# Kernel tuning notes

Hardware: AMD Instinct MI355X
Metric: run time of the kernel (lower is better)

Reference implementation:

```python
import jax, jax.numpy as jnp
import numpy as np

B, D_IN, D_H, D_OUT, E = 4096, 1024, 4096, 1024, 8
N_ACTIVE = 5              # max(1, int(8 * 0.625))
TEMP = float(np.e)        # BoltzmannGate default temperature
N_CAMP_A = E // 2


def setup_inputs() -> dict:
    key = jax.random.key(0)
    ks = jax.random.split(key, 6)
    s_in = 1.0 / np.sqrt(D_IN)
    s_h = 1.0 / np.sqrt(D_H)
    return {
        "x": jax.random.normal(ks[0], (B, D_IN), jnp.float32),
        "gate_w": jax.random.normal(ks[1], (D_IN, E), jnp.float32) * s_in,
        "gate_b": jnp.zeros((E,), jnp.float32),
        "w1": jax.random.normal(ks[2], (E, D_IN, D_H), jnp.float32) * s_in,
        "b1": jnp.zeros((E, D_H), jnp.float32),
        "w2": jax.random.normal(ks[3], (E, D_H, D_OUT), jnp.float32) * s_h,
        "b2": jnp.zeros((E, D_OUT), jnp.float32),
        "ph_alpha": jnp.array(1.0, jnp.float32),
        "ph_beta": jnp.array(0.0, jnp.float32),
    }


def _forward(x, gate_w, gate_b, w1, b1, w2, b2, ph_alpha, ph_beta):
    # BoltzmannGate: softmax over temperature-scaled scores, top-k mask, renorm
    scores = (x @ gate_w + gate_b) / TEMP                 # [B, E]
    probs = jax.nn.softmax(scores, axis=-1)
    _, topk_idx = jax.lax.top_k(probs, N_ACTIVE)          # [B, k]
    rows = jnp.arange(x.shape[0])[:, None]
    mask = jnp.zeros_like(probs).at[rows, topk_idx].set(1.0)
    w = probs * mask
    weights = w / (w.sum(axis=-1, keepdims=True) + 1e-8)  # [B, E]

    # Dense evaluation of all experts (dropout is inference-mode identity)
    h = jax.nn.relu(jnp.einsum("bi,eih->beh", x, w1) + b1)     # [B, E, H]
    e_out = jnp.einsum("beh,eho->beo", h, w2) + b2             # [B, E, O]

    # Camp A = experts [0, E//2), Camp G = experts [E//2, E)
    out_a = jnp.einsum("be,beo->bo", weights[:, :N_CAMP_A], e_out[:, :N_CAMP_A])
    out_g = jnp.einsum("be,beo->bo", weights[:, N_CAMP_A:], e_out[:, N_CAMP_A:])

    repulsion = out_a - out_g
    # PH distance proxy computed on detached tensors in torch -> stop_gradient
    diff = jax.lax.stop_gradient(repulsion)
    l2 = jnp.linalg.norm(diff, axis=-1)                   # [B]
    var = jnp.var(diff, axis=-1)                          # population var, ddof=0
    ph_dist = l2 * (1.0 + var)
    ph_corr = jax.nn.sigmoid(ph_alpha * ph_dist + ph_beta) * 2.0  # in (0, 2)
    output = repulsion * ph_corr[:, None]
    return output, out_a, out_g


def reference(x, gate_w, gate_b, w1, b1, w2, b2, ph_alpha, ph_beta):
    return _forward(x, gate_w, gate_b, w1, b1, w2, b2, ph_alpha, ph_beta)
```

## Files before the change

kernel.cpp:

```cpp
#include <hip/hip_runtime.h>
#include <hip/hip_bf16.h>
#include <stdint.h>

typedef unsigned short u16;
typedef unsigned int u32;
typedef __attribute__((ext_vector_type(4))) float f32x4;
typedef __attribute__((ext_vector_type(4))) int i32x4;
typedef __attribute__((ext_vector_type(8))) u16 u16x8;
typedef __attribute__((ext_vector_type(8))) __bf16 bf16x8;

constexpr int BATCH = 4096, DIN = 1024, DH = 4096, DOUT = 1024, NEXP = 8;
constexpr int HS_CAP = 2816;

struct Ptr4 { float* p[4]; };

__device__ __forceinline__ u16 f2bf(float f) {
  u32 u = __float_as_uint(f);
  u += 0x7fffu + ((u >> 16) & 1u);
  return (u16)(u >> 16);
}

#define GLOAD_LDS16(gp, lp)                                                    \
  __builtin_amdgcn_global_load_lds(                                           \
      (__attribute__((address_space(1))) void*)(gp),                          \
      (__attribute__((address_space(3))) void*)(lp), 16, 0, 0)

#define BAR()                                                                  \
  { asm volatile("" ::: "memory"); __builtin_amdgcn_s_barrier();               \
    asm volatile("" ::: "memory"); }
#define VM4() asm volatile("s_waitcnt vmcnt(4)" ::: "memory")
#define VM0() asm volatile("s_waitcnt vmcnt(0)" ::: "memory")

#define STG4(q0, q1, kofs, dst)                                                \
  { GLOAD_LDS16((q0) + (kofs), (dst));                                         \
    GLOAD_LDS16((q1) + (kofs), (dst) + 4096); }

__global__ void gate_kernel(const float* __restrict__ x,
                            const float* __restrict__ gw,
                            const float* __restrict__ gb,
                            float* __restrict__ wgt) {
  const int wave = threadIdx.x >> 6, lane = threadIdx.x & 63;
  const int b = blockIdx.x * 4 + wave;
  const float* xr = x + (size_t)b * DIN;
  float acc[NEXP];
#pragma unroll
  for (int e = 0; e < NEXP; ++e) acc[e] = 0.f;
  for (int k = lane; k < DIN; k += 64) {
    const float xv = xr[k];
    const f32x4 g0 = *(const f32x4*)(gw + (size_t)k * NEXP);
    const f32x4 g1 = *(const f32x4*)(gw + (size_t)k * NEXP + 4);
    acc[0] += xv * g0[0]; acc[1] += xv * g0[1];
    acc[2] += xv * g0[2]; acc[3] += xv * g0[3];
    acc[4] += xv * g1[0]; acc[5] += xv * g1[1];
    acc[6] += xv * g1[2]; acc[7] += xv * g1[3];
  }
#pragma unroll
  for (int off = 32; off; off >>= 1)
#pragma unroll
    for (int e = 0; e < NEXP; ++e) acc[e] += __shfl_xor(acc[e], off);
  if (lane == 0) {
    const float invT = 0.36787944117144233f;
    float s[NEXP], mx = -1e30f;
    for (int e = 0; e < NEXP; ++e) { s[e] = (acc[e] + gb[e]) * invT; mx = fmaxf(mx, s[e]); }
    float p[NEXP], sum = 0.f;
    for (int e = 0; e < NEXP; ++e) { p[e] = expf(s[e] - mx); sum += p[e]; }
    const float inv = 1.f / sum;
    for (int e = 0; e < NEXP; ++e) p[e] *= inv;
    float w[NEXP], wsum = 0.f;
    for (int e = 0; e < NEXP; ++e) {
      int cnt = 0;
      for (int j = 0; j < NEXP; ++j) cnt += (p[j] > p[e]) || (p[j] == p[e] && j < e);
      w[e] = (cnt < 5) ? p[e] : 0.f;
      wsum += w[e];
    }
    const float inv2 = 1.f / (wsum + 1e-8f);
    for (int e = 0; e < NEXP; ++e) wgt[(size_t)b * NEXP + e] = w[e] * inv2;
  }
}

__global__ void assign_kernel(const float* __restrict__ wgt,
                              int* __restrict__ cnt, u16* __restrict__ ridx) {
  const int b = blockIdx.x * 256 + threadIdx.x;
#pragma unroll
  for (int e = 0; e < NEXP; ++e) {
    if (wgt[(size_t)b * NEXP + e] != 0.f) {
      const int pos = atomicAdd(&cnt[e], 1);
      if (pos < BATCH) ridx[e * BATCH + pos] = (u16)b;
    }
  }
}

__global__ void gather_cvt(const float* __restrict__ x,
                           const int* __restrict__ cnt,
                           const u16* __restrict__ ridx,
                           u16* __restrict__ Xe) {
  const int e = blockIdx.y, p = blockIdx.x;
  int c = cnt[e]; c = c < HS_CAP ? c : HS_CAP;
  if (p >= c) return;
  const int row = ridx[e * BATCH + p];
  const float* s = x + (size_t)row * DIN;
  u16* d = Xe + ((size_t)e * HS_CAP + p) * DIN;
  const int t = threadIdx.x;
  const f32x4 a = *(const f32x4*)(s + t * 8);
  const f32x4 b = *(const f32x4*)(s + t * 8 + 4);
  u16x8 o;
  o[0] = f2bf(a[0]); o[1] = f2bf(a[1]); o[2] = f2bf(a[2]); o[3] = f2bf(a[3]);
  o[4] = f2bf(b[0]); o[5] = f2bf(b[1]); o[6] = f2bf(b[2]); o[7] = f2bf(b[3]);
  *(u16x8*)(d + t * 8) = o;
}

__global__ void transpose_cvt(const float* __restrict__ src, u16* __restrict__ dst,
                              int C, int ldd, size_t src_slice,
                              size_t dst_hi, size_t dst_lo) {
  __shared__ float ts[64][65];
  const int z = blockIdx.z;
  const float* s = src + (size_t)z * src_slice;
  u16* d = dst + (size_t)(z >> 2) * dst_hi + (size_t)(z & 3) * dst_lo;
  const int c0 = blockIdx.x * 64, r0 = blockIdx.y * 64;
  const int t = threadIdx.x;
  const int lr = t >> 4, lc = (t & 15) * 4;
#pragma unroll
  for (int i = 0; i < 4; ++i) {
    const f32x4 v = *(const f32x4*)(s + (size_t)(r0 + i * 16 + lr) * C + c0 + lc);
    ts[i * 16 + lr][lc] = v[0];
    ts[i * 16 + lr][lc + 1] = v[1];
    ts[i * 16 + lr][lc + 2] = v[2];
    ts[i * 16 + lr][lc + 3] = v[3];
  }
  __syncthreads();
  const int cc = t >> 3, r8 = (t & 7) * 8;
#pragma unroll
  for (int pass = 0; pass < 2; ++pass) {
    const int c = cc + pass * 32;
    u16x8 o;
#pragma unroll
    for (int j = 0; j < 8; ++j) o[j] = f2bf(ts[r8 + j][c]);
    *(u16x8*)(d + (size_t)(c0 + c) * ldd + r0 + r8) = o;
  }
}

__device__ __forceinline__ void rdB4(i32x4 rB[2][2], const char* base, int wc,
                                     int roff, int NH) {
#pragma unroll
  for (int n = 0; n < 2; ++n)
#pragma unroll
    for (int kk = 0; kk < 2; ++kk)
      rB[n][kk] = *(const i32x4*)(base + (((wc * 4 + NH * 2 + n) * 2 + kk) << 10) + roff);
}
template <int MH>
__device__ __forceinline__ void rdA8(i32x4 rA[4][2], const char* base, int wr, int roff) {
#pragma unroll
  for (int m = 0; m < 4; ++m)
#pragma unroll
    for (int kk = 0; kk < 2; ++kk)
      rA[m][kk] = *(const i32x4*)(base + (((wr * 8 + MH * 4 + m) * 2 + kk) << 10) + roff);
}
template <int MH, int NH>
__device__ __forceinline__ void mm16(f32x4 acc[8][4], const i32x4 rA[4][2],
                                     const i32x4 rB[2][2]) {
  __builtin_amdgcn_s_setprio(1);
#pragma unroll
  for (int m = 0; m < 4; ++m)
#pragma unroll
    for (int n = 0; n < 2; ++n)
#pragma unroll
      for (int kk = 0; kk < 2; ++kk)
        acc[MH * 4 + m][NH * 2 + n] = __builtin_amdgcn_mfma_f32_16x16x32_bf16(
            __builtin_bit_cast(bf16x8, rA[m][kk]),
            __builtin_bit_cast(bf16x8, rB[n][kk]),
            acc[MH * 4 + m][NH * 2 + n], 0, 0, 0);
  __builtin_amdgcn_s_setprio(0);
}

#define TILE_BODY(T, CA, CB_, DA_OT, DB_CB)                                    \
  {                                                                            \
    const int t_ = (T);                                                        \
    const bool g1 = (t_ + 1) < NT, g2 = (t_ + 2) < NT;                         \
    const int kA = (t_ + 1) * 64, kB = (t_ + 2) * 64;                          \
    rdA8<0>(rA, CA, wr, roff);                                                 \
    rdB4(rB0, CB_, wc, roff, 0);                                               \
    if (g1) STG4(qA0, qA1, kA, DA_OT);                                         \
    BAR();                                                                     \
    mm16<0, 0>(acc, rA, rB0);                                                  \
    BAR();                                                                     \
    rdB4(rB1, CB_, wc, roff, 1);                                               \
    if (g1) STG4(qA2, qA3, kA, DA_OT + 8192);                                  \
    BAR();                                                                     \
    mm16<0, 1>(acc, rA, rB1);                                                  \
    BAR();                                                                     \
    rdA8<1>(rA, CA, wr, roff);                                                 \
    if (g2) STG4(qB0, qB1, kB, DB_CB);                                         \
    BAR();                                                                     \
    mm16<1, 1>(acc, rA, rB1);                                                  \
    BAR();                                                                     \
    if (g2) {                                                                  \
      STG4(qB2, qB3, kB, DB_CB + 8192);                                        \
      BAR();                                                                   \
      mm16<1, 0>(acc, rA, rB0);                                                \
      VM4();                                                                   \
    } else {                                                                   \
      BAR();                                                                   \
      mm16<1, 0>(acc, rA, rB0);                                                \
      VM0();                                                                   \
    }                                                                          \
    BAR();                                                                     \
  }

template <int EPI>
__global__ __launch_bounds__(512, 2) void gemm256(
    const u16* __restrict__ A0, int lda,
    const u16* __restrict__ Bt0, int ldb, int K,
    u16* __restrict__ dstH0, Ptr4 parts,
    const float* __restrict__ wgt, const float* __restrict__ bias0,
    const int* __restrict__ cnt, const u16* __restrict__ ridx, int camp,
    int NM, int NN) {
  __shared__ __align__(16) u16 sA[2][16384];
  __shared__ __align__(16) u16 sB[2][16384];

  const int tid = threadIdx.x;
  const int w = tid >> 6, lane = tid & 63;
  const int l15 = lane & 15, lh = lane >> 4;
  const int wr = w >> 2, wc = w & 3;

  const int cpx = (int)gridDim.x >> 3;
  const int id = blockIdx.x;
  const int wk = (id & 7) * cpx + (id >> 3);
  const int m = wk % NM;
  const int n = (wk / NM) % NN;
  const int z = wk / (NM * NN);
  const int bM = m * 256, bN = n * 256;

  const int expert = camp * 4 + z;
  int count = cnt[expert];
  count = count < HS_CAP ? count : HS_CAP;
  if (bM >= count) return;
  const int eoff = expert * BATCH;

  const u16* A;
  const u16* Bt;
  const float* bias = bias0;
  u16* dstH = dstH0;
  if (EPI == 0) {
    A = A0 + (size_t)expert * HS_CAP * lda;
    Bt = Bt0 + (size_t)expert * DH * DIN;
    bias = bias0 + (size_t)expert * DH;
    dstH = dstH0 + (size_t)z * HS_CAP * DH;
  } else {
    A = A0 + (size_t)z * HS_CAP * lda;
    Bt = Bt0 + (size_t)z * DH;
  }

  const int lp = lane ^ ((lane & 32) >> 4);
  const int grow = (w >> 1) * 16 + (lp >> 2);
  const int gcol = (w & 1) * 32 + (lp & 3) * 8;

  const u16* qA0 = A + (size_t)(bM + grow) * lda + gcol;
  const u16* qA1 = qA0 + (size_t)64 * lda;
  const u16* qA2 = qA0 + (size_t)128 * lda;
  const u16* qA3 = qA0 + (size_t)192 * lda;
  const u16* qB0 = Bt + (size_t)(bN + grow) * ldb + gcol;
  const u16* qB1 = qB0 + (size_t)64 * ldb;
  const u16* qB2 = qB0 + (size_t)128 * ldb;
  const u16* qB3 = qB0 + (size_t)192 * ldb;

  u16* dA0 = &sA[0][w * 512];
  u16* dA1 = &sA[1][w * 512];
  u16* dB0 = &sB[0][w * 512];
  u16* dB1 = &sB[1][w * 512];

  const int roff = l15 * 64 + ((lh * 16) ^ ((l15 & 8) << 2));
  const char* cA0 = (const char*)&sA[0][0];
  const char* cA1 = (const char*)&sA[1][0];
  const char* cB0 = (const char*)&sB[0][0];
  const char* cB1 = (const char*)&sB[1][0];

  const int NT = K >> 6;
  f32x4 acc[8][4] = {};
  i32x4 rA[4][2], rB0[2][2], rB1[2][2];

  STG4(qB0, qB1, 0, dB0);
  STG4(qB2, qB3, 0, dB0 + 8192);
  STG4(qA0, qA1, 0, dA0);
  STG4(qA2, qA3, 0, dA0 + 8192);
  STG4(qB0, qB1, 64, dB1);
  STG4(qB2, qB3, 64, dB1 + 8192);
  VM4();
  BAR();

  for (int t = 0; t < NT; t += 2) {
    TILE_BODY(t, cA0, cB0, dA1, dB0);
    TILE_BODY(t + 1, cA1, cB1, dA0, dB1);
  }

  if (EPI == 0) {
#pragma unroll
    for (int m2 = 0; m2 < 8; ++m2)
#pragma unroll
      for (int r = 0; r < 4; ++r) {
        const int pos = bM + wr * 128 + m2 * 16 + lh * 4 + r;
        if (pos >= count) continue;
        const int orow = ridx[eoff + pos];
        const float wsc = wgt[(size_t)orow * NEXP + expert];
#pragma unroll
        for (int nn = 0; nn < 4; ++nn) {
          const int col = bN + wc * 64 + nn * 16 + l15;
          float v = acc[m2][nn][r] + bias[col];
          v = fmaxf(v, 0.0f) * wsc;
          dstH[(size_t)pos * DH + col] = f2bf(v);
        }
      }
  } else {
    float* __restrict__ P = parts.p[z];
#pragma unroll
    for (int m2 = 0; m2 < 8; ++m2)
#pragma unroll
      for (int r = 0; r < 4; ++r) {
        const int pos = bM + wr * 128 + m2 * 16 + lh * 4 + r;
        if (pos >= count) continue;
        const int orow = ridx[eoff + pos];
#pragma unroll
        for (int nn = 0; nn < 4; ++nn) {
          const int col = bN + wc * 64 + nn * 16 + l15;
          P[(size_t)orow * DOUT + col] = acc[m2][nn][r];
        }
      }
  }
}

__global__ __launch_bounds__(512, 2) void gemm_combo(
    const u16* __restrict__ Hs0, const u16* __restrict__ w2t0, Ptr4 pc0,
    const u16* __restrict__ Xe, const u16* __restrict__ w1t,
    u16* __restrict__ HsW, const float* __restrict__ b1,
    const float* __restrict__ wgt,
    const int* __restrict__ cnt, const u16* __restrict__ ridx, int l2n) {
  __shared__ __align__(16) u16 sA[2][16384];
  __shared__ __align__(16) u16 sB[2][16384];

  const int tid = threadIdx.x;
  const int w = tid >> 6, lane = tid & 63;
  const int l15 = lane & 15, lh = lane >> 4;
  const int wr = w >> 2, wc = w & 3;

  const bool isL2 = (int)blockIdx.x < l2n;
  const int id = isL2 ? (int)blockIdx.x : (int)blockIdx.x - l2n;
  const int tot = isL2 ? l2n : ((int)gridDim.x - l2n);
  const int cpx = tot >> 3;
  const int wk = (id & 7) * cpx + (id >> 3);
  const int NM = HS_CAP / 256;
  const int NN = isL2 ? (DOUT / 256) : (DH / 256);
  const int m = wk % NM;
  const int n = (wk / NM) % NN;
  const int z = wk / (NM * NN);
  const int bM = m * 256, bN = n * 256;

  const int expert = isL2 ? z : 4 + z;
  int count = cnt[expert];
  count = count < HS_CAP ? count : HS_CAP;
  if (bM >= count) return;
  const int eoff = expert * BATCH;

  const u16* A; const u16* Bt;
  int lda, ldb, K;
  const float* bias = nullptr;
  u16* dstH = nullptr;
  if (isL2) {
    A = Hs0 + (size_t)z * HS_CAP * DH;  lda = DH;
    Bt = w2t0 + (size_t)z * DH;         ldb = 4 * DH;
    K = DH;
  } else {
    A = Xe + (size_t)expert * HS_CAP * DIN;  lda = DIN;
    Bt = w1t + (size_t)expert * DH * DIN;    ldb = DIN;
    K = DIN;
    bias = b1 + (size_t)expert * DH;
    dstH = HsW + (size_t)expert * HS_CAP * DH;
  }

  const int lp = lane ^ ((lane & 32) >> 4);
  const int grow = (w >> 1) * 16 + (lp >> 2);
  const int gcol = (w & 1) * 32 + (lp & 3) * 8;

  const u16* qA0 = A + (size_t)(bM + grow) * lda + gcol;
  const u16* qA1 = qA0 + (size_t)64 * lda;
  const u16* qA2 = qA0 + (size_t)128 * lda;
  const u16* qA3 = qA0 + (size_t)192 * lda;
  const u16* qB0 = Bt + (size_t)(bN + grow) * ldb + gcol;
  const u16* qB1 = qB0 + (size_t)64 * ldb;
  const u16* qB2 = qB0 + (size_t)128 * ldb;
  const u16* qB3 = qB0 + (size_t)192 * ldb;

  u16* dA0 = &sA[0][w * 512];
  u16* dA1 = &sA[1][w * 512];
  u16* dB0 = &sB[0][w * 512];
  u16* dB1 = &sB[1][w * 512];

  const int roff = l15 * 64 + ((lh * 16) ^ ((l15 & 8) << 2));
  const char* cA0 = (const char*)&sA[0][0];
  const char* cA1 = (const char*)&sA[1][0];
  const char* cB0 = (const char*)&sB[0][0];
  const char* cB1 = (const char*)&sB[1][0];

  const int NT = K >> 6;
  f32x4 acc[8][4] = {};
  i32x4 rA[4][2], rB0[2][2], rB1[2][2];

  STG4(qB0, qB1, 0, dB0);
  STG4(qB2, qB3, 0, dB0 + 8192);
  STG4(qA0, qA1, 0, dA0);
  STG4(qA2, qA3, 0, dA0 + 8192);
  STG4(qB0, qB1, 64, dB1);
  STG4(qB2, qB3, 64, dB1 + 8192);
  VM4();
  BAR();

  for (int t = 0; t < NT; t += 2) {
    TILE_BODY(t, cA0, cB0, dA1, dB0);
    TILE_BODY(t + 1, cA1, cB1, dA0, dB1);
  }

  if (isL2) {
    float* __restrict__ P = pc0.p[z];
#pragma unroll
    for (int m2 = 0; m2 < 8; ++m2)
#pragma unroll
      for (int r = 0; r < 4; ++r) {
        const int pos = bM + wr * 128 + m2 * 16 + lh * 4 + r;
        if (pos >= count) continue;
        const int orow = ridx[eoff + pos];
#pragma unroll
        for (int nn = 0; nn < 4; ++nn) {
          const int col = bN + wc * 64 + nn * 16 + l15;
          P[(size_t)orow * DOUT + col] = acc[m2][nn][r];
        }
      }
  } else {
#pragma unroll
    for (int m2 = 0; m2 < 8; ++m2)
#pragma unroll
      for (int r = 0; r < 4; ++r) {
        const int pos = bM + wr * 128 + m2 * 16 + lh * 4 + r;
        if (pos >= count) continue;
        const int orow = ridx[eoff + pos];
        const float wsc = wgt[(size_t)orow * NEXP + expert];
#pragma unroll
        for (int nn = 0; nn < 4; ++nn) {
          const int col = bN + wc * 64 + nn * 16 + l15;
          float v = acc[m2][nn][r] + bias[col];
          v = fmaxf(v, 0.0f) * wsc;
          dstH[(size_t)pos * DH + col] = f2bf(v);
        }
      }
  }
}

__global__ void reduce_kernel(float* __restrict__ dst,
                              const float* __restrict__ p0, const float* __restrict__ p1,
                              const float* __restrict__ p2, const float* __restrict__ p3,
                              const float* __restrict__ wgt,
                              const float* __restrict__ b2c, int camp) {
  const int b = blockIdx.x, t = threadIdx.x;
  const f32x4 wv = *(const f32x4*)(wgt + (size_t)b * NEXP + camp * 4);
  const size_t ro = (size_t)b * DOUT;
#pragma unroll
  for (int j = 0; j < 4; ++j) {
    const int i = j * 256 + t;
    float acc = wv[0] * b2c[i] + wv[1] * b2c[DOUT + i] +
                wv[2] * b2c[2 * DOUT + i] + wv[3] * b2c[3 * DOUT + i];
    acc += (wv[0] != 0.f) ? p0[ro + i] : 0.f;
    acc += (wv[1] != 0.f) ? p1[ro + i] : 0.f;
    acc += (wv[2] != 0.f) ? p2[ro + i] : 0.f;
    acc += (wv[3] != 0.f) ? p3[ro + i] : 0.f;
    dst[ro + i] = acc;
  }
}

__global__ void reduce_final_kernel(float* __restrict__ out,
                                    const float* __restrict__ p0,
                                    const float* __restrict__ p1,
                                    const float* __restrict__ p2,
                                    const float* __restrict__ p3,
                                    const float* __restrict__ wgt,
                                    const float* __restrict__ b2c,
                                    const float* __restrict__ alpha,
                                    const float* __restrict__ beta) {
  const int b = blockIdx.x, t = threadIdx.x;
  const f32x4 wv = *(const f32x4*)(wgt + (size_t)b * NEXP + 4);
  const size_t ro = (size_t)b * DOUT;
  const float* pa = out + (size_t)BATCH * DOUT + ro;
  float* pg = out + (size_t)2 * BATCH * DOUT + ro;
  float* po = out + ro;
  float g[4], d[4], s1 = 0.f, s2 = 0.f;
#pragma unroll
  for (int j = 0; j < 4; ++j) {
    const int i = j * 256 + t;
    float acc = wv[0] * b2c[i] + wv[1] * b2c[DOUT + i] +
                wv[2] * b2c[2 * DOUT + i] + wv[3] * b2c[3 * DOUT + i];
    acc += (wv[0] != 0.f) ? p0[ro + i] : 0.f;
    acc += (wv[1] != 0.f) ? p1[ro + i] : 0.f;
    acc += (wv[2] != 0.f) ? p2[ro + i] : 0.f;
    acc += (wv[3] != 0.f) ? p3[ro + i] : 0.f;
    g[j] = acc;
    d[j] = pa[i] - acc;
    s1 += d[j];
    s2 += d[j] * d[j];
  }
#pragma unroll
  for (int off = 32; off; off >>= 1) {
    s1 += __shfl_xor(s1, off);
    s2 += __shfl_xor(s2, off);
  }
  __shared__ float r1[4], r2[4];
  if ((t & 63) == 0) { r1[t >> 6] = s1; r2[t >> 6] = s2; }
  __syncthreads();
  s1 = r1[0] + r1[1] + r1[2] + r1[3];
  s2 = r2[0] + r2[1] + r2[2] + r2[3];
  const float mean = s1 * (1.f / DOUT);
  const float var = s2 * (1.f / DOUT) - mean * mean;
  const float dist = sqrtf(s2) * (1.f + var);
  const float zz = alpha[0] * dist + beta[0];
  const float corr = 2.f / (1.f + expf(-zz));
#pragma unroll
  for (int j = 0; j < 4; ++j) {
    const int i = j * 256 + t;
    pg[i] = g[j];
    po[i] = d[j] * corr;
  }
}

extern "C" void kernel_launch(void* const* d_in, const int* in_sizes, int n_in,
                              void* d_out, int out_size, void* d_ws, size_t ws_size,
                              hipStream_t stream) {
  const float* x   = (const float*)d_in[0];
  const float* gw  = (const float*)d_in[1];
  const float* gb  = (const float*)d_in[2];
  const float* w1  = (const float*)d_in[3];
  const float* b1  = (const float*)d_in[4];
  const float* w2  = (const float*)d_in[5];
  const float* b2  = (const float*)d_in[6];
  const float* pha = (const float*)d_in[7];
  const float* phb = (const float*)d_in[8];
  float* out = (float*)d_out;
  float* out_a = out + (size_t)BATCH * DOUT;
  float* out_g = out + (size_t)2 * BATCH * DOUT;

  char* ws = (char*)d_ws;
  float* wgt  = (float*)ws;
  int* cnt    = (int*)(ws + 131072);
  u16* ridx   = (u16*)(ws + 135168);
  u16* Xe     = (u16*)(ws + 262144);
  constexpr size_t XE_BYTES  = (size_t)NEXP * HS_CAP * DIN * 2;
  constexpr size_t W1T_BYTES = (size_t)NEXP * DH * DIN * 2;
  constexpr size_t W2T_BYTES = (size_t)DOUT * 4 * DH * 2;
  constexpr size_t P_BYTES   = (size_t)BATCH * DOUT * 4;
  constexpr size_t HS_E      = (size_t)HS_CAP * DH * 2;
  const size_t w1t_off = 262144 + XE_BYTES;
  u16* w1t = (u16*)(ws + w1t_off);

  const size_t pipe_need = w1t_off + W1T_BYTES + 2 * W2T_BYTES + 2 * P_BYTES + 8 * HS_E;
  const size_t merged_need = w1t_off + W1T_BYTES + 2 * P_BYTES + 8 * HS_E;

  constexpr int NM = HS_CAP / 256;
  constexpr int NN1 = DH / 256, NN2 = DOUT / 256;

  gate_kernel<<<BATCH / 4, 256, 0, stream>>>(x, gw, gb, wgt);
  hipMemsetAsync(cnt, 0, NEXP * sizeof(int), stream);
  assign_kernel<<<BATCH / 256, 256, 0, stream>>>(wgt, cnt, ridx);
  gather_cvt<<<dim3(HS_CAP, NEXP), 128, 0, stream>>>(x, cnt, ridx, Xe);
  transpose_cvt<<<dim3(DH / 64, DIN / 64, NEXP), 256, 0, stream>>>(
      w1, w1t, DH, DIN, (size_t)DIN * DH, (size_t)4 * DH * DIN, (size_t)DH * DIN);

  if (ws_size >= pipe_need) {
    u16* w2t0 = (u16*)(ws + w1t_off + W1T_BYTES);
    u16* w2t1 = (u16*)(ws + w1t_off + W1T_BYTES + W2T_BYTES);
    float* P0 = (float*)(ws + w1t_off + W1T_BYTES + 2 * W2T_BYTES);
    float* P1 = (float*)(ws + w1t_off + W1T_BYTES + 2 * W2T_BYTES + P_BYTES);
    u16* Hs   = (u16*)(ws + w1t_off + W1T_BYTES + 2 * W2T_BYTES + 2 * P_BYTES);
    Ptr4 pc0 = {{out_a, out, out_g, P0}};
    Ptr4 pc1 = {{out_g, out, P0, P1}};

    transpose_cvt<<<dim3(DOUT / 64, DH / 64, 4), 256, 0, stream>>>(
        w2, w2t0, DOUT, 4 * DH, (size_t)DH * DOUT, 0, (size_t)DH);
    transpose_cvt<<<dim3(DOUT / 64, DH / 64, 4), 256, 0, stream>>>(
        w2 + (size_t)4 * DH * DOUT, w2t1, DOUT, 4 * DH, (size_t)DH * DOUT, 0, (size_t)DH);

    gemm256<0><<<NM * NN1 * 4, 512, 0, stream>>>(
        Xe, DIN, w1t, DIN, DIN, Hs, pc0, wgt, b1, cnt, ridx, 0, NM, NN1);
    gemm_combo<<<NM * NN2 * 4 + NM * NN1 * 4, 512, 0, stream>>>(
        Hs, w2t0, pc0, Xe, w1t, Hs, b1, wgt, cnt, ridx, NM * NN2 * 4);
    reduce_kernel<<<BATCH, 256, 0, stream>>>(out_a, out_a, out, out_g, P0, wgt, b2, 0);
    gemm256<2><<<NM * NN2 * 4, 512, 0, stream>>>(
        Hs + (size_t)4 * HS_CAP * DH, DH, w2t1, 4 * DH, DH, nullptr, pc1,
        nullptr, nullptr, cnt, ridx, 1, NM, NN2);
    reduce_final_kernel<<<BATCH, 256, 0, stream>>>(out, out_g, out, P0, P1,
                                                   wgt, b2 + (size_t)4 * DOUT,
                                                   pha, phb);
  } else if (ws_size >= merged_need) {
    float* P0 = (float*)(ws + w1t_off + W1T_BYTES);
    float* P1 = (float*)(ws + w1t_off + W1T_BYTES + P_BYTES);
    u16* Hs   = (u16*)(ws + w1t_off + W1T_BYTES + 2 * P_BYTES);
    u16* w2t0 = w1t;
    u16* w2t1 = (u16*)((char*)w1t + W2T_BYTES);
    Ptr4 pc0 = {{out_a, out, out_g, P0}};
    Ptr4 pc1 = {{out_g, out, P0, P1}};

    gemm256<0><<<NM * NN1 * 8, 512, 0, stream>>>(
        Xe, DIN, w1t, DIN, DIN, Hs, pc0, wgt, b1, cnt, ridx, 0, NM, NN1);
    transpose_cvt<<<dim3(DOUT / 64, DH / 64, 4), 256, 0, stream>>>(
        w2, w2t0, DOUT, 4 * DH, (size_t)DH * DOUT, 0, (size_t)DH);
    transpose_cvt<<<dim3(DOUT / 64, DH / 64, 4), 256, 0, stream>>>(
        w2 + (size_t)4 * DH * DOUT, w2t1, DOUT, 4 * DH, (size_t)DH * DOUT, 0, (size_t)DH);
    gemm256<2><<<NM * NN2 * 4, 512, 0, stream>>>(
        Hs, DH, w2t0, 4 * DH, DH, nullptr, pc0, nullptr, nullptr, cnt, ridx, 0, NM, NN2);
    reduce_kernel<<<BATCH, 256, 0, stream>>>(out_a, out_a, out, out_g, P0, wgt, b2, 0);
    gemm256<2><<<NM * NN2 * 4, 512, 0, stream>>>(
        Hs + (size_t)4 * HS_CAP * DH, DH, w2t1, 4 * DH, DH, nullptr, pc1,
        nullptr, nullptr, cnt, ridx, 1, NM, NN2);
    reduce_final_kernel<<<BATCH, 256, 0, stream>>>(out, out_g, out, P0, P1,
                                                   wgt, b2 + (size_t)4 * DOUT,
                                                   pha, phb);
  } else {
    u16* w2t1 = w1t;
    u16* w2t0 = (u16*)(ws + w1t_off + W1T_BYTES);
    float* P0 = (float*)(ws + w1t_off + W1T_BYTES + W2T_BYTES);
    float* P1 = (float*)(ws + w1t_off + W1T_BYTES + W2T_BYTES + P_BYTES);
    u16* Hs   = (u16*)(ws + w1t_off + W1T_BYTES + W2T_BYTES + 2 * P_BYTES);
    Ptr4 pc0 = {{out_a, out, out_g, P0}};
    Ptr4 pc1 = {{out_g, out, P0, P1}};

    transpose_cvt<<<dim3(DOUT / 64, DH / 64, 4), 256, 0, stream>>>(
        w2, w2t0, DOUT, 4 * DH, (size_t)DH * DOUT, 0, (size_t)DH);
    gemm256<0><<<NM * NN1 * 4, 512, 0, stream>>>(
        Xe, DIN, w1t, DIN, DIN, Hs, pc0, wgt, b1, cnt, ridx, 0, NM, NN1);
    transpose_cvt<<<dim3(DOUT / 64, DH / 64, 4), 256, 0, stream>>>(
        w2 + (size_t)4 * DH * DOUT, w2t1, DOUT, 4 * DH, (size_t)DH * DOUT, 0, (size_t)DH);
    gemm256<2><<<NM * NN2 * 4, 512, 0, stream>>>(
        Hs, DH, w2t0, 4 * DH, DH, nullptr, pc0, nullptr, nullptr, cnt, ridx, 0, NM, NN2);
    reduce_kernel<<<BATCH, 256, 0, stream>>>(out_a, out_a, out, out_g, P0, wgt, b2, 0);
    gemm256<0><<<NM * NN1 * 4, 512, 0, stream>>>(
        Xe, DIN, w1t, DIN, DIN, Hs, pc1, wgt, b1, cnt, ridx, 1, NM, NN1);
    gemm256<2><<<NM * NN2 * 4, 512, 0, stream>>>(
        Hs, DH, w2t1, 4 * DH, DH, nullptr, pc1, nullptr, nullptr, cnt, ridx, 1, NM, NN2);
    reduce_final_kernel<<<BATCH, 256, 0, stream>>>(out, out_g, out, P0, P1,
                                                   wgt, b2 + (size_t)4 * DOUT,
                                                   pha, phb);
  }
}
```

Before: 650.8 us.

## Fuse prep stages and overlap weight transposes with GEMMs in heterogeneous launches

Folds expert assignment into the gate kernel and merges the gather/convert with the w1 transpose into one heterogeneous launch. The w2 transpose now runs in the same launch as the layer-1 GEMM, and the camp-A reduce runs alongside the camp-G layer-2 GEMM. The w2 transpose also moves to 512-thread blocks that each handle two tiles, and scratch buffers are remapped onto dead workspace. The goal is fewer launches and filling idle CUs during the GEMM tails, at the cost of more complex block dispatch and heavier LDS use in the transpose blocks.

```diff
diff --git a/kernel.cpp b/kernel.cpp
--- a/kernel.cpp
+++ b/kernel.cpp
@@ -38,7 +38,8 @@
 __global__ void gate_kernel(const float* __restrict__ x,
                             const float* __restrict__ gw,
                             const float* __restrict__ gb,
-                            float* __restrict__ wgt) {
+                            float* __restrict__ wgt,
+                            int* __restrict__ cnt, u16* __restrict__ ridx) {
   const int wave = threadIdx.x >> 6, lane = threadIdx.x & 63;
   const int b = blockIdx.x * 4 + wave;
   const float* xr = x + (size_t)b * DIN;
@@ -68,75 +69,91 @@
     for (int e = 0; e < NEXP; ++e) p[e] *= inv;
     float w[NEXP], wsum = 0.f;
     for (int e = 0; e < NEXP; ++e) {
-      int cnt = 0;
-      for (int j = 0; j < NEXP; ++j) cnt += (p[j] > p[e]) || (p[j] == p[e] && j < e);
-      w[e] = (cnt < 5) ? p[e] : 0.f;
+      int c = 0;
+      for (int j = 0; j < NEXP; ++j) c += (p[j] > p[e]) || (p[j] == p[e] && j < e);
+      w[e] = (c < 5) ? p[e] : 0.f;
       wsum += w[e];
     }
     const float inv2 = 1.f / (wsum + 1e-8f);
-    for (int e = 0; e < NEXP; ++e) wgt[(size_t)b * NEXP + e] = w[e] * inv2;
-  }
-}
-
-__global__ void assign_kernel(const float* __restrict__ wgt,
-                              int* __restrict__ cnt, u16* __restrict__ ridx) {
-  const int b = blockIdx.x * 256 + threadIdx.x;
-#pragma unroll
-  for (int e = 0; e < NEXP; ++e) {
-    if (wgt[(size_t)b * NEXP + e] != 0.f) {
-      const int pos = atomicAdd(&cnt[e], 1);
-      if (pos < BATCH) ridx[e * BATCH + pos] = (u16)b;
+    for (int e = 0; e < NEXP; ++e) {
+      const float wv = w[e] * inv2;
+      wgt[(size_t)b * NEXP + e] = wv;
+      if (wv != 0.f) {
+        const int pos = atomicAdd(&cnt[e], 1);
+        if (pos < BATCH) ridx[e * BATCH + pos] = (u16)b;
+      }
     }
   }
 }
 
-__global__ void gather_cvt(const float* __restrict__ x,
-                           const int* __restrict__ cnt,
-                           const u16* __restrict__ ridx,
-                           u16* __restrict__ Xe) {
-  const int e = blockIdx.y, p = blockIdx.x;
+__device__ __forceinline__ void transpose_pair(
+    const float* __restrict__ src, u16* __restrict__ dst, int C, int ldd,
+    size_t src_slice, size_t dst_hi, size_t dst_lo, int id, int nc2, int nr,
+    float* ts ) {
+  const int tid = threadIdx.x;
+  const int half = tid >> 8, t = tid & 255;
+  const int cp = id % nc2;
+  const int rt = (id / nc2) % nr;
+  const int z = id / (nc2 * nr);
+  const float* s = src + (size_t)z * src_slice;
+  u16* d = dst + (size_t)(z >> 2) * dst_hi + (size_t)(z & 3) * dst_lo;
+  const int c0 = cp * 128 + half * 64, r0 = rt * 64;
+  float* th = ts + half * (64 * 65);
+  const int lr = t >> 4, lc = (t & 15) * 4;
+#pragma unroll
+  for (int i = 0; i < 4; ++i) {
+    const f32x4 v = *(const f32x4*)(s + (size_t)(r0 + i * 16 + lr) * C + c0 + lc);
+    th[(i * 16 + lr) * 65 + lc] = v[0];
+    th[(i * 16 + lr) * 65 + lc + 1] = v[1];
+    th[(i * 16 + lr) * 65 + lc + 2] = v[2];
+    th[(i * 16 + lr) * 65 + lc + 3] = v[3];
+  }
+  __syncthreads();
+  const int cc = t >> 3, r8 = (t & 7) * 8;
+#pragma unroll
+  for (int pass = 0; pass < 2; ++pass) {
+    const int c = cc + pass * 32;
+    u16x8 o;
+#pragma unroll
+    for (int j = 0; j < 8; ++j) o[j] = f2bf(th[(r8 + j) * 65 + c]);
+    *(u16x8*)(d + (size_t)(c0 + c) * ldd + r0 + r8) = o;
+  }
+}
+
+__global__ __launch_bounds__(512) void transpose_pair_kernel(
+    const float* __restrict__ src, u16* __restrict__ dst, int C, int ldd,
+    size_t src_slice, size_t dst_hi, size_t dst_lo, int nc2, int nr) {
+  __shared__ float ts[2][64][65];
+  transpose_pair(src, dst, C, ldd, src_slice, dst_hi, dst_lo, blockIdx.x, nc2,
+                 nr, &ts[0][0][0]);
+}
+
+__global__ __launch_bounds__(512) void prep_hetero(
+    const float* __restrict__ x, const int* __restrict__ cnt,
+    const u16* __restrict__ ridx, u16* __restrict__ Xe,
+    const float* __restrict__ w1, u16* __restrict__ w1t, int gn) {
+  __shared__ float ts[2][64][65];
+  const int id = blockIdx.x;
+  if (id >= gn) {
+    transpose_pair(w1, w1t, DH, DIN, (size_t)DIN * DH, (size_t)4 * DH * DIN,
+                   (size_t)DH * DIN, id - gn, DH / 128, DIN / 64, &ts[0][0][0]);
+    return;
+  }
+  const int tid = threadIdx.x;
+  const int e = id / (HS_CAP / 4);
+  const int p = (id % (HS_CAP / 4)) * 4 + (tid >> 7);
   int c = cnt[e]; c = c < HS_CAP ? c : HS_CAP;
   if (p >= c) return;
   const int row = ridx[e * BATCH + p];
   const float* s = x + (size_t)row * DIN;
   u16* d = Xe + ((size_t)e * HS_CAP + p) * DIN;
-  const int t = threadIdx.x;
+  const int t = tid & 127;
   const f32x4 a = *(const f32x4*)(s + t * 8);
   const f32x4 b = *(const f32x4*)(s + t * 8 + 4);
   u16x8 o;
   o[0] = f2bf(a[0]); o[1] = f2bf(a[1]); o[2] = f2bf(a[2]); o[3] = f2bf(a[3]);
   o[4] = f2bf(b[0]); o[5] = f2bf(b[1]); o[6] = f2bf(b[2]); o[7] = f2bf(b[3]);
   *(u16x8*)(d + t * 8) = o;
-}
-
-__global__ void transpose_cvt(const float* __restrict__ src, u16* __restrict__ dst,
-                              int C, int ldd, size_t src_slice,
-                              size_t dst_hi, size_t dst_lo) {
-  __shared__ float ts[64][65];
-  const int z = blockIdx.z;
-  const float* s = src + (size_t)z * src_slice;
-  u16* d = dst + (size_t)(z >> 2) * dst_hi + (size_t)(z & 3) * dst_lo;
-  const int c0 = blockIdx.x * 64, r0 = blockIdx.y * 64;
-  const int t = threadIdx.x;
-  const int lr = t >> 4, lc = (t & 15) * 4;
-#pragma unroll
-  for (int i = 0; i < 4; ++i) {
-    const f32x4 v = *(const f32x4*)(s + (size_t)(r0 + i * 16 + lr) * C + c0 + lc);
-    ts[i * 16 + lr][lc] = v[0];
-    ts[i * 16 + lr][lc + 1] = v[1];
-    ts[i * 16 + lr][lc + 2] = v[2];
-    ts[i * 16 + lr][lc + 3] = v[3];
-  }
-  __syncthreads();
-  const int cc = t >> 3, r8 = (t & 7) * 8;
-#pragma unroll
-  for (int pass = 0; pass < 2; ++pass) {
-    const int c = cc + pass * 32;
-    u16x8 o;
-#pragma unroll
-    for (int j = 0; j < 8; ++j) o[j] = f2bf(ts[r8 + j][c]);
-    *(u16x8*)(d + (size_t)(c0 + c) * ldd + r0 + r8) = o;
-  }
 }
 
 __device__ __forceinline__ void rdB4(i32x4 rB[2][2], const char* base, int wc,
@@ -206,6 +223,50 @@
     BAR();                                                                     \
   }
 
+#define GEMM_COORDS()                                                          \
+  const int tid = threadIdx.x;                                                 \
+  const int w = tid >> 6, lane = tid & 63;                                     \
+  const int l15 = lane & 15, lh = lane >> 4;                                   \
+  const int wr = w >> 2, wc = w & 3;                                           \
+  const int lp = lane ^ ((lane & 32) >> 4);                                    \
+  const int grow = (w >> 1) * 16 + (lp >> 2);                                  \
+  const int gcol = (w & 1) * 32 + (lp & 3) * 8;                                \
+  const int roff = l15 * 64 + ((lh * 16) ^ ((l15 & 8) << 2));                  \
+  const char* cA0 = (const char*)&sA[0][0];                                    \
+  const char* cA1 = (const char*)&sA[1][0];                                    \
+  const char* cB0 = (const char*)&sB[0][0];                                    \
+  const char* cB1 = (const char*)&sB[1][0];                                    \
+  u16* dA0 = &sA[0][w * 512];                                                  \
+  u16* dA1 = &sA[1][w * 512];                                                  \
+  u16* dB0 = &sB[0][w * 512];                                                  \
+  u16* dB1 = &sB[1][w * 512];
+
+#define GEMM_POINTERS(A, lda, Bt, ldb)                                         \
+  const u16* qA0 = (A) + (size_t)(bM + grow) * (lda) + gcol;                   \
+  const u16* qA1 = qA0 + (size_t)64 * (lda);                                   \
+  const u16* qA2 = qA0 + (size_t)128 * (lda);                                  \
+  const u16* qA3 = qA0 + (size_t)192 * (lda);                                  \
+  const u16* qB0 = (Bt) + (size_t)(bN + grow) * (ldb) + gcol;                  \
+  const u16* qB1 = qB0 + (size_t)64 * (ldb);                                   \
+  const u16* qB2 = qB0 + (size_t)128 * (ldb);                                  \
+  const u16* qB3 = qB0 + (size_t)192 * (ldb);
+
+#define GEMM_RUN()                                                             \
+  f32x4 acc[8][4] = {};                                                        \
+  i32x4 rA[4][2], rB0[2][2], rB1[2][2];                                        \
+  STG4(qB0, qB1, 0, dB0);                                                      \
+  STG4(qB2, qB3, 0, dB0 + 8192);                                               \
+  STG4(qA0, qA1, 0, dA0);                                                      \
+  STG4(qA2, qA3, 0, dA0 + 8192);                                               \
+  STG4(qB0, qB1, 64, dB1);                                                     \
+  STG4(qB2, qB3, 64, dB1 + 8192);                                              \
+  VM4();                                                                       \
+  BAR();                                                                       \
+  for (int t = 0; t < NT; t += 2) {                                            \
+    TILE_BODY(t, cA0, cB0, dA1, dB0);                                          \
+    TILE_BODY(t + 1, cA1, cB1, dA0, dB1);                                      \
+  }
+
 template <int EPI>
 __global__ __launch_bounds__(512, 2) void gemm256(
     const u16* __restrict__ A0, int lda,
@@ -216,11 +277,7 @@
     int NM, int NN) {
   __shared__ __align__(16) u16 sA[2][16384];
   __shared__ __align__(16) u16 sB[2][16384];
-
-  const int tid = threadIdx.x;
-  const int w = tid >> 6, lane = tid & 63;
-  const int l15 = lane & 15, lh = lane >> 4;
-  const int wr = w >> 2, wc = w & 3;
+  GEMM_COORDS();
 
   const int cpx = (int)gridDim.x >> 3;
   const int id = blockIdx.x;
@@ -249,48 +306,9 @@
     A = A0 + (size_t)z * HS_CAP * lda;
     Bt = Bt0 + (size_t)z * DH;
   }
-
-  const int lp = lane ^ ((lane & 32) >> 4);
-  const int grow = (w >> 1) * 16 + (lp >> 2);
-  const int gcol = (w & 1) * 32 + (lp & 3) * 8;
-
-  const u16* qA0 = A + (size_t)(bM + grow) * lda + gcol;
-  const u16* qA1 = qA0 + (size_t)64 * lda;
-  const u16* qA2 = qA0 + (size_t)128 * lda;
-  const u16* qA3 = qA0 + (size_t)192 * lda;
-  const u16* qB0 = Bt + (size_t)(bN + grow) * ldb + gcol;
-  const u16* qB1 = qB0 + (size_t)64 * ldb;
-  const u16* qB2 = qB0 + (size_t)128 * ldb;
-  const u16* qB3 = qB0 + (size_t)192 * ldb;
-
-  u16* dA0 = &sA[0][w * 512];
-  u16* dA1 = &sA[1][w * 512];
-  u16* dB0 = &sB[0][w * 512];
-  u16* dB1 = &sB[1][w * 512];
-
-  const int roff = l15 * 64 + ((lh * 16) ^ ((l15 & 8) << 2));
-  const char* cA0 = (const char*)&sA[0][0];
-  const char* cA1 = (const char*)&sA[1][0];
-  const char* cB0 = (const char*)&sB[0][0];
-  const char* cB1 = (const char*)&sB[1][0];
-
+  GEMM_POINTERS(A, lda, Bt, ldb);
   const int NT = K >> 6;
-  f32x4 acc[8][4] = {};
-  i32x4 rA[4][2], rB0[2][2], rB1[2][2];
-
-  STG4(qB0, qB1, 0, dB0);
-  STG4(qB2, qB3, 0, dB0 + 8192);
-  STG4(qA0, qA1, 0, dA0);
-  STG4(qA2, qA3, 0, dA0 + 8192);
-  STG4(qB0, qB1, 64, dB1);
-  STG4(qB2, qB3, 64, dB1 + 8192);
-  VM4();
-  BAR();
-
-  for (int t = 0; t < NT; t += 2) {
-    TILE_BODY(t, cA0, cB0, dA1, dB0);
-    TILE_BODY(t + 1, cA1, cB1, dA0, dB1);
-  }
+  GEMM_RUN();
 
   if (EPI == 0) {
 #pragma unroll
@@ -327,6 +345,63 @@
   }
 }
 
+__global__ __launch_bounds__(512, 2) void l1_w2t_hetero(
+    const u16* __restrict__ Xe, const u16* __restrict__ w1t,
+    u16* __restrict__ Hs, const float* __restrict__ wgt,
+    const float* __restrict__ b1,
+    const int* __restrict__ cnt, const u16* __restrict__ ridx,
+    const float* __restrict__ w2, u16* __restrict__ w2t0, int l1n) {
+  __shared__ __align__(16) u16 sA[2][16384];
+  __shared__ __align__(16) u16 sB[2][16384];
+  if ((int)blockIdx.x >= l1n) {
+    transpose_pair(w2, w2t0, DOUT, 4 * DH, (size_t)DH * DOUT,
+                   (size_t)DOUT * 4 * DH, (size_t)DH,
+                   (int)blockIdx.x - l1n, DOUT / 128, DH / 64,
+                   (float*)&sA[0][0]);
+    return;
+  }
+  GEMM_COORDS();
+  const int NM = HS_CAP / 256, NN = DH / 256;
+  const int cpx = l1n >> 3;
+  const int id = blockIdx.x;
+  const int wk = (id & 7) * cpx + (id >> 3);
+  const int m = wk % NM;
+  const int n = (wk / NM) % NN;
+  const int z = wk / (NM * NN);
+  const int bM = m * 256, bN = n * 256;
+
+  const int expert = z;
+  int count = cnt[expert];
+  count = count < HS_CAP ? count : HS_CAP;
+  if (bM >= count) return;
+  const int eoff = expert * BATCH;
+
+  const u16* A = Xe + (size_t)expert * HS_CAP * DIN;
+  const u16* Bt = w1t + (size_t)expert * DH * DIN;
+  const float* bias = b1 + (size_t)expert * DH;
+  u16* dstH = Hs + (size_t)expert * HS_CAP * DH;
+  GEMM_POINTERS(A, DIN, Bt, DIN);
+  constexpr int NT = DIN >> 6;
+  GEMM_RUN();
+
+#pragma unroll
+  for (int m2 = 0; m2 < 8; ++m2)
+#pragma unroll
+    for (int r = 0; r < 4; ++r) {
+      const int pos = bM + wr * 128 + m2 * 16 + lh * 4 + r;
+      if (pos >= count) continue;
+      const int orow = ridx[eoff + pos];
+      const float wsc = wgt[(size_t)orow * NEXP + expert];
+#pragma unroll
+      for (int nn = 0; nn < 4; ++nn) {
+        const int col = bN + wc * 64 + nn * 16 + l15;
+        float v = acc[m2][nn][r] + bias[col];
+        v = fmaxf(v, 0.0f) * wsc;
+        dstH[(size_t)pos * DH + col] = f2bf(v);
+      }
+    }
+}
+
 __global__ __launch_bounds__(512, 2) void gemm_combo(
     const u16* __restrict__ Hs0, const u16* __restrict__ w2t0, Ptr4 pc0,
     const u16* __restrict__ Xe, const u16* __restrict__ w1t,
@@ -335,11 +410,7 @@
     const int* __restrict__ cnt, const u16* __restrict__ ridx, int l2n) {
   __shared__ __align__(16) u16 sA[2][16384];
   __shared__ __align__(16) u16 sB[2][16384];
-
-  const int tid = threadIdx.x;
-  const int w = tid >> 6, lane = tid & 63;
-  const int l15 = lane & 15, lh = lane >> 4;
-  const int wr = w >> 2, wc = w & 3;
+  GEMM_COORDS();
 
   const bool isL2 = (int)blockIdx.x < l2n;
   const int id = isL2 ? (int)blockIdx.x : (int)blockIdx.x - l2n;
@@ -374,48 +445,9 @@
     bias = b1 + (size_t)expert * DH;
     dstH = HsW + (size_t)expert * HS_CAP * DH;
   }
-
-  const int lp = lane ^ ((lane & 32) >> 4);
-  const int grow = (w >> 1) * 16 + (lp >> 2);
-  const int gcol = (w & 1) * 32 + (lp & 3) * 8;
-
-  const u16* qA0 = A + (size_t)(bM + grow) * lda + gcol;
-  const u16* qA1 = qA0 + (size_t)64 * lda;
-  const u16* qA2 = qA0 + (size_t)128 * lda;
-  const u16* qA3 = qA0 + (size_t)192 * lda;
-  const u16* qB0 = Bt + (size_t)(bN + grow) * ldb + gcol;
-  const u16* qB1 = qB0 + (size_t)64 * ldb;
-  const u16* qB2 = qB0 + (size_t)128 * ldb;
-  const u16* qB3 = qB0 + (size_t)192 * ldb;
-
-  u16* dA0 = &sA[0][w * 512];
-  u16* dA1 = &sA[1][w * 512];
-  u16* dB0 = &sB[0][w * 512];
-  u16* dB1 = &sB[1][w * 512];
-
-  const int roff = l15 * 64 + ((lh * 16) ^ ((l15 & 8) << 2));
-  const char* cA0 = (const char*)&sA[0][0];
-  const char* cA1 = (const char*)&sA[1][0];
-  const char* cB0 = (const char*)&sB[0][0];
-  const char* cB1 = (const char*)&sB[1][0];
-
+  GEMM_POINTERS(A, lda, Bt, ldb);
   const int NT = K >> 6;
-  f32x4 acc[8][4] = {};
-  i32x4 rA[4][2], rB0[2][2], rB1[2][2];
-
-  STG4(qB0, qB1, 0, dB0);
-  STG4(qB2, qB3, 0, dB0 + 8192);
-  STG4(qA0, qA1, 0, dA0);
-  STG4(qA2, qA3, 0, dA0 + 8192);
-  STG4(qB0, qB1, 64, dB1);
-  STG4(qB2, qB3, 64, dB1 + 8192);
-  VM4();
-  BAR();
-
-  for (int t = 0; t < NT; t += 2) {
-    TILE_BODY(t, cA0, cB0, dA1, dB0);
-    TILE_BODY(t + 1, cA1, cB1, dA0, dB1);
-  }
+  GEMM_RUN();
 
   if (isL2) {
     float* __restrict__ P = pc0.p[z];
@@ -450,6 +482,71 @@
         }
       }
   }
+}
+
+__global__ __launch_bounds__(512, 2) void l2_red_hetero(
+    const u16* __restrict__ Hs4, const u16* __restrict__ w2t1, Ptr4 pc1,
+    float* __restrict__ ra_dst,
+    const float* __restrict__ q0, const float* __restrict__ q1,
+    const float* __restrict__ q2, const float* __restrict__ q3,
+    const float* __restrict__ wgt, const float* __restrict__ b2c0,
+    const int* __restrict__ cnt, const u16* __restrict__ ridx, int l2n) {
+  __shared__ __align__(16) u16 sA[2][16384];
+  __shared__ __align__(16) u16 sB[2][16384];
+  if ((int)blockIdx.x >= l2n) {
+    const int t = threadIdx.x & 255;
+    const int b = ((int)blockIdx.x - l2n) * 2 + (threadIdx.x >> 8);
+    const f32x4 wv = *(const f32x4*)(wgt + (size_t)b * NEXP);
+    const size_t ro = (size_t)b * DOUT;
+#pragma unroll
+    for (int j = 0; j < 4; ++j) {
+      const int i = j * 256 + t;
+      float acc = wv[0] * b2c0[i] + wv[1] * b2c0[DOUT + i] +
+                  wv[2] * b2c0[2 * DOUT + i] + wv[3] * b2c0[3 * DOUT + i];
+      acc += (wv[0] != 0.f) ? q0[ro + i] : 0.f;
+      acc += (wv[1] != 0.f) ? q1[ro + i] : 0.f;
+      acc += (wv[2] != 0.f) ? q2[ro + i] : 0.f;
+      acc += (wv[3] != 0.f) ? q3[ro + i] : 0.f;
+      ra_dst[ro + i] = acc;
+    }
+    return;
+  }
+  GEMM_COORDS();
+  const int NM = HS_CAP / 256, NN = DOUT / 256;
+  const int cpx = l2n >> 3;
+  const int id = blockIdx.x;
+  const int wk = (id & 7) * cpx + (id >> 3);
+  const int m = wk % NM;
+  const int n = (wk / NM) % NN;
+  const int z = wk / (NM * NN);
+  const int bM = m * 256, bN = n * 256;
+
+  const int expert = 4 + z;
+  int count = cnt[expert];
+  count = count < HS_CAP ? count : HS_CAP;
+  if (bM >= count) return;
+  const int eoff = expert * BATCH;
+
+  const u16* A = Hs4 + (size_t)z * HS_CAP * DH;
+  const u16* Bt = w2t1 + (size_t)z * DH;
+  GEMM_POINTERS(A, DH, Bt, 4 * DH);
+  constexpr int NT = DH >> 6;
+  GEMM_RUN();
+
+  float* __restrict__ P = pc1.p[z];
+#pragma unroll
+  for (int m2 = 0; m2 < 8; ++m2)
+#pragma unroll
+    for (int r = 0; r < 4; ++r) {
+      const int pos = bM + wr * 128 + m2 * 16 + lh * 4 + r;
+      if (pos >= count) continue;
+      const int orow = ridx[eoff + pos];
+#pragma unroll
+      for (int nn = 0; nn < 4; ++nn) {
+        const int col = bN + wc * 64 + nn * 16 + l15;
+        P[(size_t)orow * DOUT + col] = acc[m2][nn][r];
+      }
+    }
 }
 
 __global__ void reduce_kernel(float* __restrict__ dst,
@@ -560,13 +657,13 @@
 
   constexpr int NM = HS_CAP / 256;
   constexpr int NN1 = DH / 256, NN2 = DOUT / 256;
-
-  gate_kernel<<<BATCH / 4, 256, 0, stream>>>(x, gw, gb, wgt);
+  constexpr int GN = NEXP * (HS_CAP / 4);
+  constexpr int W1TB = (DH / 128) * (DIN / 64) * NEXP;
+  constexpr int W2TB = (DOUT / 128) * (DH / 64) * NEXP;
+
   hipMemsetAsync(cnt, 0, NEXP * sizeof(int), stream);
-  assign_kernel<<<BATCH / 256, 256, 0, stream>>>(wgt, cnt, ridx);
-  gather_cvt<<<dim3(HS_CAP, NEXP), 128, 0, stream>>>(x, cnt, ridx, Xe);
-  transpose_cvt<<<dim3(DH / 64, DIN / 64, NEXP), 256, 0, stream>>>(
-      w1, w1t, DH, DIN, (size_t)DIN * DH, (size_t)4 * DH * DIN, (size_t)DH * DIN);
+  gate_kernel<<<BATCH / 4, 256, 0, stream>>>(x, gw, gb, wgt, cnt, ridx);
+  prep_hetero<<<GN + W1TB, 512, 0, stream>>>(x, cnt, ridx, Xe, w1, w1t, GN);
 
   if (ws_size >= pipe_need) {
     u16* w2t0 = (u16*)(ws + w1t_off + W1T_BYTES);
@@ -574,25 +671,21 @@
     float* P0 = (float*)(ws + w1t_off + W1T_BYTES + 2 * W2T_BYTES);
     float* P1 = (float*)(ws + w1t_off + W1T_BYTES + 2 * W2T_BYTES + P_BYTES);
     u16* Hs   = (u16*)(ws + w1t_off + W1T_BYTES + 2 * W2T_BYTES + 2 * P_BYTES);
+    float* F0 = (float*)w1t;
+    float* F1 = (float*)((char*)w1t + P_BYTES);
+    float* F2 = (float*)Xe;
     Ptr4 pc0 = {{out_a, out, out_g, P0}};
-    Ptr4 pc1 = {{out_g, out, P0, P1}};
-
-    transpose_cvt<<<dim3(DOUT / 64, DH / 64, 4), 256, 0, stream>>>(
-        w2, w2t0, DOUT, 4 * DH, (size_t)DH * DOUT, 0, (size_t)DH);
-    transpose_cvt<<<dim3(DOUT / 64, DH / 64, 4), 256, 0, stream>>>(
-        w2 + (size_t)4 * DH * DOUT, w2t1, DOUT, 4 * DH, (size_t)DH * DOUT, 0, (size_t)DH);
-
-    gemm256<0><<<NM * NN1 * 4, 512, 0, stream>>>(
-        Xe, DIN, w1t, DIN, DIN, Hs, pc0, wgt, b1, cnt, ridx, 0, NM, NN1);
+    Ptr4 pc1 = {{F0, F1, F2, P1}};
+
+    l1_w2t_hetero<<<NM * NN1 * 4 + W2TB, 512, 0, stream>>>(
+        Xe, w1t, Hs, wgt, b1, cnt, ridx, w2, w2t0, NM * NN1 * 4);
     gemm_combo<<<NM * NN2 * 4 + NM * NN1 * 4, 512, 0, stream>>>(
         Hs, w2t0, pc0, Xe, w1t, Hs, b1, wgt, cnt, ridx, NM * NN2 * 4);
-    reduce_kernel<<<BATCH, 256, 0, stream>>>(out_a, out_a, out, out_g, P0, wgt, b2, 0);
-    gemm256<2><<<NM * NN2 * 4, 512, 0, stream>>>(
-        Hs + (size_t)4 * HS_CAP * DH, DH, w2t1, 4 * DH, DH, nullptr, pc1,
-        nullptr, nullptr, cnt, ridx, 1, NM, NN2);
-    reduce_final_kernel<<<BATCH, 256, 0, stream>>>(out, out_g, out, P0, P1,
-                                                   wgt, b2 + (size_t)4 * DOUT,
-                                                   pha, phb);
+    l2_red_hetero<<<NM * NN2 * 4 + BATCH / 2, 512, 0, stream>>>(
+        Hs + (size_t)4 * HS_CAP * DH, w2t1, pc1, out_a, out_a, out, out_g, P0,
+        wgt, b2, cnt, ridx, NM * NN2 * 4);
+    reduce_final_kernel<<<BATCH, 256, 0, stream>>>(out, F0, F1, F2, P1, wgt,
+                                                   b2 + (size_t)4 * DOUT, pha, phb);
   } else if (ws_size >= merged_need) {
     float* P0 = (float*)(ws + w1t_off + W1T_BYTES);
     float* P1 = (float*)(ws + w1t_off + W1T_BYTES + P_BYTES);
@@ -604,19 +697,17 @@
 
     gemm256<0><<<NM * NN1 * 8, 512, 0, stream>>>(
         Xe, DIN, w1t, DIN, DIN, Hs, pc0, wgt, b1, cnt, ridx, 0, NM, NN1);
-    transpose_cvt<<<dim3(DOUT / 64, DH / 64, 4), 256, 0, stream>>>(
-        w2, w2t0, DOUT, 4 * DH, (size_t)DH * DOUT, 0, (size_t)DH);
-    transpose_cvt<<<dim3(DOUT / 64, DH / 64, 4), 256, 0, stream>>>(
-        w2 + (size_t)4 * DH * DOUT, w2t1, DOUT, 4 * DH, (size_t)DH * DOUT, 0, (size_t)DH);
+    transpose_pair_kernel<<<W2TB, 512, 0, stream>>>(
+        w2, w2t0, DOUT, 4 * DH, (size_t)DH * DOUT, (size_t)DOUT * 4 * DH,
+        (size_t)DH, DOUT / 128, DH / 64);
     gemm256<2><<<NM * NN2 * 4, 512, 0, stream>>>(
         Hs, DH, w2t0, 4 * DH, DH, nullptr, pc0, nullptr, nullptr, cnt, ridx, 0, NM, NN2);
     reduce_kernel<<<BATCH, 256, 0, stream>>>(out_a, out_a, out, out_g, P0, wgt, b2, 0);
     gemm256<2><<<NM * NN2 * 4, 512, 0, stream>>>(
         Hs + (size_t)4 * HS_CAP * DH, DH, w2t1, 4 * DH, DH, nullptr, pc1,
         nullptr, nullptr, cnt, ridx, 1, NM, NN2);
-    reduce_final_kernel<<<BATCH, 256, 0, stream>>>(out, out_g, out, P0, P1,
-                                                   wgt, b2 + (size_t)4 * DOUT,
-                                                   pha, phb);
+    reduce_final_kernel<<<BATCH, 256, 0, stream>>>(out, out_g, out, P0, P1, wgt,
+                                                   b2 + (size_t)4 * DOUT, pha, phb);
   } else {
     u16* w2t1 = w1t;
     u16* w2t0 = (u16*)(ws + w1t_off + W1T_BYTES);
@@ -626,12 +717,14 @@
     Ptr4 pc0 = {{out_a, out, out_g, P0}};
     Ptr4 pc1 = {{out_g, out, P0, P1}};
 
-    transpose_cvt<<<dim3(DOUT / 64, DH / 64, 4), 256, 0, stream>>>(
-        w2, w2t0, DOUT, 4 * DH, (size_t)DH * DOUT, 0, (size_t)DH);
+    transpose_pair_kernel<<<W2TB / 2, 512, 0, stream>>>(
+        w2, w2t0, DOUT, 4 * DH, (size_t)DH * DOUT, 0, (size_t)DH,
+        DOUT / 128, DH / 64);
     gemm256<0><<<NM * NN1 * 4, 512, 0, stream>>>(
         Xe, DIN, w1t, DIN, DIN, Hs, pc0, wgt, b1, cnt, ridx, 0, NM, NN1);
-    transpose_cvt<<<dim3(DOUT / 64, DH / 64, 4), 256, 0, stream>>>(
-        w2 + (size_t)4 * DH * DOUT, w2t1, DOUT, 4 * DH, (size_t)DH * DOUT, 0, (size_t)DH);
+    transpose_pair_kernel<<<W2TB / 2, 512, 0, stream>>>(
+        w2 + (size_t)4 * DH * DOUT, w2t1, DOUT, 4 * DH, (size_t)DH * DOUT, 0,
+        (size_t)DH, DOUT / 128, DH / 64);
     gemm256<2><<<NM * NN2 * 4, 512, 0, stream>>>(
         Hs, DH, w2t0, 4 * DH, DH, nullptr, pc0, nullptr, nullptr, cnt, ridx, 0, NM, NN2);
     reduce_kernel<<<BATCH, 256, 0, stream>>>(out_a, out_a, out, out_g, P0, wgt, b2, 0);
@@ -639,8 +732,7 @@
         Xe, DIN, w1t, DIN, DIN, Hs, pc1, wgt, b1, cnt, ridx, 1, NM, NN1);
     gemm256<2><<<NM * NN2 * 4, 512, 0, stream>>>(
         Hs, DH, w2t1, 4 * DH, DH, nullptr, pc1, nullptr, nullptr, cnt, ridx, 1, NM, NN2);
-    reduce_final_kernel<<<BATCH, 256, 0, stream>>>(out, out_g, out, P0, P1,
-                                                   wgt, b2 + (size_t)4 * DOUT,
-                                                   pha, phb);
-  }
-}
+    reduce_final_kernel<<<BATCH, 256, 0, stream>>>(out, out_g, out, P0, P1, wgt,
+                                                   b2 + (size_t)4 * DOUT, pha, phb);
+  }
+}
```

Measured after the change: 838.9 us. +28.9%, slower.
